# Kernel tuning notes

Hardware: AMD Instinct MI355X
Metric: run time of the kernel (lower is better)

Reference implementation:

```python
import jax, jax.numpy as jnp
import numpy as np

D_MODEL = 768
NUM_HEADS = 12
HEAD_DIM = D_MODEL // NUM_HEADS


def setup_inputs() -> dict:
    key = jax.random.key(0)
    ks = jax.random.split(key, 9)
    B, S = 2, 2048
    s = 1.0 / np.sqrt(D_MODEL)
    x = jax.random.normal(ks[0], (B, S, D_MODEL), dtype=jnp.float32)
    Wq = jax.random.normal(ks[1], (D_MODEL, D_MODEL), dtype=jnp.float32) * s
    Wk = jax.random.normal(ks[2], (D_MODEL, D_MODEL), dtype=jnp.float32) * s
    Wv = jax.random.normal(ks[3], (D_MODEL, D_MODEL), dtype=jnp.float32) * s
    Wo = jax.random.normal(ks[4], (D_MODEL, D_MODEL), dtype=jnp.float32) * s
    bq = jax.random.normal(ks[5], (D_MODEL,), dtype=jnp.float32) * 0.01
    bk = jax.random.normal(ks[6], (D_MODEL,), dtype=jnp.float32) * 0.01
    bv = jax.random.normal(ks[7], (D_MODEL,), dtype=jnp.float32) * 0.01
    bo = jax.random.normal(ks[8], (D_MODEL,), dtype=jnp.float32) * 0.01
    return {"x": x, "Wq": Wq, "bq": bq, "Wk": Wk, "bk": bk,
            "Wv": Wv, "bv": bv, "Wo": Wo, "bo": bo}


def reference(x, Wq, bq, Wk, bk, Wv, bv, Wo, bo):
    B, S, _ = x.shape
    # projections; reshape to [B, H, S, Dh]
    def split_heads(t):
        return t.reshape(B, S, NUM_HEADS, HEAD_DIM).transpose(0, 2, 1, 3)
    q = split_heads(x @ Wq + bq)
    k = split_heads(x @ Wk + bk)
    v = split_heads(x @ Wv + bv)
    scale = 1.0 / np.sqrt(HEAD_DIM)
    scores = jnp.einsum("bhqd,bhkd->bhqk", q, k) * scale  # [B,H,S,S]
    attn = jax.nn.softmax(scores, axis=-1)
    # dropout p=0.0 (eval) -> identity
    ctx = jnp.einsum("bhqk,bhkd->bhqd", attn, v)
    ctx = ctx.transpose(0, 2, 1, 3).reshape(B, S, D_MODEL)
    return ctx @ Wo + bo
```

## Files before the change

### kernel.cpp

```cpp
#include <hip/hip_runtime.h>
#include <hip/hip_bf16.h>
#include <hip/hip_fp16.h>

#define D_MODEL 768
#define NHEADS  12
#define HD      64
#define BATCH   2
#define SEQ     2048
#define NTOK    (BATCH*SEQ)
#define NX      ((size_t)NTOK * D_MODEL)
#define NW      ((size_t)D_MODEL * D_MODEL)
#define SC_LOG2 0.18033688f

typedef __attribute__((ext_vector_type(8))) short    short8;
typedef __attribute__((ext_vector_type(8))) _Float16 half8;
typedef __attribute__((ext_vector_type(2))) __fp16   fp16x2;
typedef __attribute__((ext_vector_type(4))) float    f32x4;

__device__ __forceinline__ float bf2f(short s) {
    union { unsigned u; float f; } c;
    c.u = ((unsigned)(unsigned short)s) << 16;
    return c.f;
}
__device__ __forceinline__ short f2bf(float f) {
    __hip_bfloat16 h = __float2bfloat16(f);
    return *(short*)&h;
}

#ifdef __has_builtin
#if __has_builtin(__builtin_amdgcn_global_load_lds)
#define HAS_GLD 1
#endif
#if __has_builtin(__builtin_amdgcn_exp2f)
#define EXP2(x) __builtin_amdgcn_exp2f(x)
#else
#define EXP2(x) exp2f(x)
#endif
#if __has_builtin(__builtin_amdgcn_cvt_pkrtz)
#define HAS_PKRTZ 1
#endif
#else
#define EXP2(x) exp2f(x)
#endif
#ifdef HAS_GLD
#define GLD16(gp, lp) __builtin_amdgcn_global_load_lds( \
    (const __attribute__((address_space(1))) void*)(gp), \
    (__attribute__((address_space(3))) void*)(lp), 16, 0, 0)
#endif

#ifdef HAS_PKRTZ
#define PKF16(a, b) __builtin_amdgcn_cvt_pkrtz((a), (b))
#else
#define PKF16(a, b) ((fp16x2){ (__fp16)(a), (__fp16)(b) })
#endif

__global__ __launch_bounds__(256) void fused_conv(
        const void* __restrict__ xin,
        const void* __restrict__ w0, const void* __restrict__ w1,
        const void* __restrict__ w2, const void* __restrict__ w3,
        const void* __restrict__ b0, const void* __restrict__ b1,
        const void* __restrict__ b2, const void* __restrict__ b3,
        short* __restrict__ xc, short* __restrict__ wt,
        short* __restrict__ bc, int* __restrict__ flag)
{
    __shared__ int red[256];
    __shared__ float T[64][65];
    const int tid = threadIdx.x;
    const int F = blockIdx.x;

    {
        const short* xs = (const short*)xin;
        int maxe = 0;
#pragma unroll
        for (int u = 0; u < 16; ++u) {
            int e = ((unsigned short)xs[tid * 16 + u] >> 7) & 0xFF;
            maxe = max(maxe, e);
        }
        red[tid] = maxe;
        __syncthreads();
        for (int s = 128; s > 0; s >>= 1) {
            if (tid < s) red[tid] = max(red[tid], red[tid + s]);
            __syncthreads();
        }
    }
    const bool isf = (red[0] > 140);

    if (F < 3072) {
        const int i = F * 256 + tid;
        if (isf) {
            float4 f = ((const float4*)xin)[i];
            short4 o = { f2bf(f.x), f2bf(f.y), f2bf(f.z), f2bf(f.w) };
            ((short4*)xc)[i] = o;
        } else {
            ((short4*)xc)[i] = ((const short4*)xin)[i];
        }
    } else if (F < 3648) {
        const int G = F - 3072;
        const int z = G / 144, rr = G % 144;
        const int k0 = (rr % 12) * 64, n0 = (rr / 12) * 64;
        const void* src = (z == 0) ? w0 : (z == 1) ? w1 : (z == 2) ? w2 : w3;
        const float sc = (z == 0) ? SC_LOG2 : 1.0f;
        const int la = tid & 15, lb = tid >> 4;
#pragma unroll
        for (int u = 0; u < 4; ++u) {
            const int kr = (lb & 3) + 4 * u + 16 * (lb >> 2);
            if (isf) {
                float4 f = *(const float4*)((const float*)src + (size_t)(k0 + kr) * D_MODEL + n0 + la * 4);
                T[kr][la*4+0] = f.x; T[kr][la*4+1] = f.y; T[kr][la*4+2] = f.z; T[kr][la*4+3] = f.w;
            } else {
                short4 s = *(const short4*)((const short*)src + (size_t)(k0 + kr) * D_MODEL + n0 + la * 4);
                T[kr][la*4+0] = bf2f(s.x); T[kr][la*4+1] = bf2f(s.y);
                T[kr][la*4+2] = bf2f(s.z); T[kr][la*4+3] = bf2f(s.w);
            }
        }
        __syncthreads();
#pragma unroll
        for (int u = 0; u < 4; ++u) {
            const int nr = (lb & 3) + 4 * u + 16 * (lb >> 2);
            short4 o = { f2bf(T[la*4+0][nr] * sc), f2bf(T[la*4+1][nr] * sc),
                         f2bf(T[la*4+2][nr] * sc), f2bf(T[la*4+3][nr] * sc) };
            *(short4*)(wt + (size_t)z * NW + (size_t)(n0 + nr) * D_MODEL + k0 + la * 4) = o;
        }
    } else {
        if (tid == 0) *flag = isf ? 1 : 0;
        const void* srcs[4] = { b0, b1, b2, b3 };
        for (int z = 0; z < 4; ++z) {
            const float sc = (z == 0) ? SC_LOG2 : 1.0f;
            for (int i = tid; i < D_MODEL; i += 256) {
                float v = isf ? ((const float*)srcs[z])[i] : bf2f(((const short*)srcs[z])[i]);
                bc[z * D_MODEL + i] = f2bf(v * sc);
            }
        }
    }
}

__global__ __launch_bounds__(256) void qkv_gemm(const short* __restrict__ X,
                                                const short* __restrict__ Wt,
                                                const short* __restrict__ bias,
                                                short* __restrict__ qb,
                                                short* __restrict__ kb,
                                                _Float16* __restrict__ Vt)
{
    __shared__ __align__(16) char shbuf[24576];
    short* Als = (short*)shbuf;
    short* Bls = (short*)(shbuf + 8192);
    _Float16* T = (_Float16*)shbuf;

    const int tid = threadIdx.x;
    const int wave = tid >> 6, lane = tid & 63;
    const int quad = lane >> 4, l16 = lane & 15;
    const int wm = wave & 1, wn = wave >> 1;
    const int m0 = blockIdx.x * 64;
    const int ng = blockIdx.y * 128;

    f32x4 acc[2][4];
#pragma unroll
    for (int nt = 0; nt < 4; ++nt) {
        const float bv = bf2f(bias[ng + wn*64 + nt*16 + l16]);
#pragma unroll
        for (int mt = 0; mt < 2; ++mt) acc[mt][nt] = (f32x4){bv, bv, bv, bv};
    }

    const int row = tid >> 2, ch = (tid & 3) * 8;
#ifdef HAS_GLD
#define QSTAGE(buf, k0) do { \
        GLD16(X  + (size_t)(m0 + row)      * D_MODEL + (k0) + ch, &Als[(buf)*2048 + tid*8]); \
        GLD16(Wt + (size_t)(ng + row)      * D_MODEL + (k0) + ch, &Bls[(buf)*4096 + tid*8]); \
        GLD16(Wt + (size_t)(ng + 64 + row) * D_MODEL + (k0) + ch, &Bls[(buf)*4096 + 2048 + tid*8]); \
    } while (0)
#else
#define QSTAGE(buf, k0) do { \
        short8 r0 = *(const short8*)(X  + (size_t)(m0 + row)      * D_MODEL + (k0) + ch); \
        short8 r2 = *(const short8*)(Wt + (size_t)(ng + row)      * D_MODEL + (k0) + ch); \
        short8 r3 = *(const short8*)(Wt + (size_t)(ng + 64 + row) * D_MODEL + (k0) + ch); \
        *(short8*)&Als[(buf)*2048 + tid*8] = r0; \
        *(short8*)&Bls[(buf)*4096 + tid*8] = r2; \
        *(short8*)&Bls[(buf)*4096 + 2048 + tid*8] = r3; \
    } while (0)
#endif

    QSTAGE(0, 0);
    __syncthreads();

    for (int ks = 0; ks < 24; ++ks) {
        const int cur = ks & 1;
        if (ks + 1 < 24) QSTAGE(cur ^ 1, (ks + 1) * 32);

        short8 a[2], b[4];
#pragma unroll
        for (int mt = 0; mt < 2; ++mt)
            a[mt] = *(const short8*)&Als[cur*2048 + (wm*32 + mt*16 + l16) * 32 + quad*8];
#pragma unroll
        for (int nt = 0; nt < 4; ++nt)
            b[nt] = *(const short8*)&Bls[cur*4096 + (wn*64 + nt*16 + l16) * 32 + quad*8];
#pragma unroll
        for (int mt = 0; mt < 2; ++mt)
#pragma unroll
        for (int nt = 0; nt < 4; ++nt)
            acc[mt][nt] = __builtin_amdgcn_mfma_f32_16x16x32_bf16(a[mt], b[nt], acc[mt][nt], 0, 0, 0);

        __syncthreads();
    }
#undef QSTAGE

    const int seg = blockIdx.y / 6;
    if (seg < 2) {
        short* out = seg ? kb : qb;
        const int nl = ng - seg * 768;
#pragma unroll
        for (int mt = 0; mt < 2; ++mt)
#pragma unroll
        for (int nt = 0; nt < 4; ++nt) {
            const int n = nl + wn*64 + nt*16 + l16;
#pragma unroll
            for (int r = 0; r < 4; ++r) {
                const int m = m0 + wm*32 + mt*16 + quad*4 + r;
                out[(size_t)m * D_MODEL + n] = f2bf(acc[mt][nt][r]);
            }
        }
    } else {
        const int batch = m0 >> 11, tokb = m0 & (SEQ - 1);
#pragma unroll
        for (int nt = 0; nt < 4; ++nt) {
            const int dim_l = wn*64 + nt*16 + l16;
#pragma unroll
            for (int mt = 0; mt < 2; ++mt) {
                const int tok_l = wm*32 + mt*16 + quad*4;
                union { _Float16 h4[4]; int2 v; } u;
#pragma unroll
                for (int r = 0; r < 4; ++r) u.h4[r] = (_Float16)acc[mt][nt][r];
                *(int2*)&T[dim_l * 72 + tok_l] = u.v;
            }
        }
        __syncthreads();
#pragma unroll
        for (int u = 0; u < 4; ++u) {
            const int slot = tid + u * 256;
            const int drow = slot >> 3, chk = slot & 7;
            int4 val = *(const int4*)&T[drow * 72 + chk * 8];
            const int dim_g = ng - 1536 + drow;
            const int h = dim_g >> 6, d = dim_g & 63;
            *(int4*)(Vt + ((size_t)(batch * NHEADS + h) * HD + d) * SEQ + tokb + chk*8) = val;
        }
    }
}

__global__ __launch_bounds__(256) void out_gemm(const short* __restrict__ X,
                                                const short* __restrict__ Wt,
                                                const short* __restrict__ bias,
                                                void* __restrict__ outv,
                                                const int* __restrict__ flag)
{
    __shared__ short Als[2][2048];
    __shared__ short Bls[2][2048];

    const int tid = threadIdx.x;
    const int wave = tid >> 6, lane = tid & 63;
    const int quad = lane >> 4, l16 = lane & 15;
    const int m0 = blockIdx.x * 64;
    const int n0 = blockIdx.y * 64;

    f32x4 acc[4];
#pragma unroll
    for (int nt = 0; nt < 4; ++nt) {
        const float bv = bf2f(bias[n0 + nt*16 + l16]);
        acc[nt] = (f32x4){bv, bv, bv, bv};
    }

    const int row = tid >> 2, ch = (tid & 3) * 8;
#ifdef HAS_GLD
#define OSTAGE(buf, k0) do { \
        GLD16(X  + (size_t)(m0 + row) * D_MODEL + (k0) + ch, &Als[buf][tid*8]); \
        GLD16(Wt + (size_t)(n0 + row) * D_MODEL + (k0) + ch, &Bls[buf][tid*8]); \
    } while (0)
#else
#define OSTAGE(buf, k0) do { \
        short8 r0 = *(const short8*)(X  + (size_t)(m0 + row) * D_MODEL + (k0) + ch); \
        short8 r1 = *(const short8*)(Wt + (size_t)(n0 + row) * D_MODEL + (k0) + ch); \
        *(short8*)&Als[buf][tid*8] = r0; \
        *(short8*)&Bls[buf][tid*8] = r1; \
    } while (0)
#endif

    OSTAGE(0, 0);
    __syncthreads();

    for (int ks = 0; ks < 24; ++ks) {
        const int cur = ks & 1;
        if (ks + 1 < 24) OSTAGE(cur ^ 1, (ks + 1) * 32);

        short8 a = *(const short8*)&Als[cur][(wave*16 + l16) * 32 + quad*8];
#pragma unroll
        for (int nt = 0; nt < 4; ++nt) {
            short8 b = *(const short8*)&Bls[cur][(nt*16 + l16) * 32 + quad*8];
            acc[nt] = __builtin_amdgcn_mfma_f32_16x16x32_bf16(a, b, acc[nt], 0, 0, 0);
        }
        __syncthreads();
    }
#undef OSTAGE

    const bool outf32 = (*flag != 0);
#pragma unroll
    for (int nt = 0; nt < 4; ++nt) {
        const int n = n0 + nt*16 + l16;
#pragma unroll
        for (int r = 0; r < 4; ++r) {
            const int m = m0 + wave*16 + quad*4 + r;
            const size_t idx = (size_t)m * D_MODEL + n;
            if (outf32) ((float*)outv)[idx] = acc[nt][r];
            else        ((short*)outv)[idx] = f2bf(acc[nt][r]);
        }
    }
}

__global__ __launch_bounds__(256, 3) void attn_mfma(const short* __restrict__ q,
                                                    const short* __restrict__ k,
                                                    const _Float16* __restrict__ Vt,
                                                    short* __restrict__ ctx)
{
    __shared__ short    Kls[2][64 * 64];
    __shared__ _Float16 Vls[3][64 * 64];
    __shared__ _Float16 Pls[4][16 * 64];

    const int tid  = threadIdx.x;
    const int wave = tid >> 6, lane = tid & 63;
    const int quad = lane >> 4, l16 = lane & 15;

    const int F = blockIdx.x;
    const int xcd = F & 7, slot = F >> 3;
    const int bh = xcd * 3 + (slot >> 5);
    const int q0 = (slot & 31) * 64;
    const int b = bh / NHEADS, h = bh % NHEADS;
    const size_t bS = (size_t)b * SEQ;
    const int myq = q0 + wave * 16 + l16;

    short8 qf[2];
#pragma unroll
    for (int k0h = 0; k0h < 2; ++k0h)
        qf[k0h] = *(const short8*)(q + (bS + myq) * D_MODEL + h*HD + k0h*32 + quad*8);

    half8 ones;
#pragma unroll
    for (int j = 0; j < 8; ++j) ones[j] = (_Float16)1.0f;

    const int s0 = tid, s1 = tid + 256;
    const int kr0 = s0 >> 3, kc0 = (s0 & 7) ^ (kr0 & 7);
    const int kr1 = s1 >> 3, kc1 = (s1 & 7) ^ (kr1 & 7);
    const short*    kg0 = k  + (bS + kr0) * D_MODEL + h*HD + kc0*8;
    const short*    kg1 = k  + (bS + kr1) * D_MODEL + h*HD + kc1*8;
    const _Float16* vg0 = Vt + ((size_t)bh * HD + kr0) * SEQ + kc0*8;
    const _Float16* vg1 = Vt + ((size_t)bh * HD + kr1) * SEQ + kc1*8;

#ifdef HAS_GLD
#define STAGE_K(buf, j0) do { \
        GLD16(kg0 + (size_t)(j0) * D_MODEL, &Kls[buf][s0 * 8]); \
        GLD16(kg1 + (size_t)(j0) * D_MODEL, &Kls[buf][s1 * 8]); \
    } while (0)
#define STAGE_V(buf, j0) do { \
        GLD16(vg0 + (j0), &Vls[buf][s0 * 8]); \
        GLD16(vg1 + (j0), &Vls[buf][s1 * 8]); \
    } while (0)
#else
#define STAGE_K(buf, j0) do { \
        short8 a_ = *(const short8*)(kg0 + (size_t)(j0) * D_MODEL); \
        short8 b_ = *(const short8*)(kg1 + (size_t)(j0) * D_MODEL); \
        *(short8*)&Kls[buf][s0 * 8] = a_;  *(short8*)&Kls[buf][s1 * 8] = b_; \
    } while (0)
#define STAGE_V(buf, j0) do { \
        half8  c_ = *(const half8*)(vg0 + (j0)); \
        half8  d_ = *(const half8*)(vg1 + (j0)); \
        *(half8*)&Vls[buf][s0 * 8] = c_;   *(half8*)&Vls[buf][s1 * 8] = d_; \
    } while (0)
#endif

    float m_ = -1e30f;
    f32x4 lacc = (f32x4){0.f, 0.f, 0.f, 0.f};
    f32x4 o[4];
#pragma unroll
    for (int t = 0; t < 4; ++t) o[t] = (f32x4){0.f, 0.f, 0.f, 0.f};

    f32x4 sA[4], sB[4];

#define QK(S, KB) do { \
    _Pragma("unroll") \
    for (int t = 0; t < 4; ++t) S[t] = (f32x4){0.f, 0.f, 0.f, 0.f}; \
    _Pragma("unroll") \
    for (int k0h = 0; k0h < 2; ++k0h) \
    _Pragma("unroll") \
    for (int t = 0; t < 4; ++t) { \
        const int krow = t*16 + l16; \
        short8 kf = *(const short8*)&Kls[KB][krow*64 + (((k0h*4 + quad) ^ (krow & 7)) * 8)]; \
        S[t] = __builtin_amdgcn_mfma_f32_16x16x32_bf16(kf, qf[k0h], S[t], 0, 0, 0); \
    } \
} while (0)

#define BODY(JT, SCUR, SNXT) do { \
    if ((JT) + 2 < SEQ/64) { \
        STAGE_K(((JT) + 2) & 1, ((JT) + 2) * 64); \
        STAGE_V(((JT) + 2) % 3, ((JT) + 2) * 64); \
    } \
    if ((JT) + 1 < SEQ/64) QK(SNXT, ((JT) + 1) & 1); \
    { \
         \
        float mx = SCUR[0][0]; \
        _Pragma("unroll") \
        for (int t = 0; t < 4; ++t) \
        _Pragma("unroll") \
        for (int r = 0; r < 4; ++r) mx = fmaxf(mx, SCUR[t][r]); \
        if (__any(mx > m_ + 8.f)) { \
            _Pragma("unroll") \
            for (int d = 1; d < 64; d <<= 1) mx = fmaxf(mx, __shfl_xor(mx, d)); \
            const float mn = fmaxf(m_, mx); \
            const float al = EXP2(m_ - mn); \
            _Pragma("unroll") \
            for (int t = 0; t < 4; ++t) { \
                o[t][0] *= al; o[t][1] *= al; o[t][2] *= al; o[t][3] *= al; \
            } \
            lacc[0] *= al; lacc[1] *= al; lacc[2] *= al; lacc[3] *= al; \
            m_ = mn; \
        } \
         \
        _Pragma("unroll") \
        for (int t = 0; t < 4; ++t) { \
            union { fp16x2 h2[2]; int2 v; } u4; \
            u4.h2[0] = PKF16(EXP2(SCUR[t][0] - m_), EXP2(SCUR[t][1] - m_)); \
            u4.h2[1] = PKF16(EXP2(SCUR[t][2] - m_), EXP2(SCUR[t][3] - m_)); \
            const int c = (t*2 + (quad >> 1)) ^ (l16 & 7); \
            *(int2*)&Pls[wave][l16*64 + c*8 + (quad & 1)*4] = u4.v; \
        } \
         \
        const int vb = (JT) % 3; \
        _Pragma("unroll") \
        for (int k0h = 0; k0h < 2; ++k0h) { \
            const int pc = (k0h*4 + quad) ^ (l16 & 7); \
            half8 pf = *(half8*)&Pls[wave][l16*64 + pc*8]; \
            lacc = __builtin_amdgcn_mfma_f32_16x16x32_f16(ones, pf, lacc, 0, 0, 0); \
            _Pragma("unroll") \
            for (int t = 0; t < 4; ++t) { \
                const int vrow = t*16 + l16; \
                half8 vf = *(const half8*)&Vls[vb][vrow*64 + (((k0h*4 + quad) ^ (vrow & 7)) * 8)]; \
                o[t] = __builtin_amdgcn_mfma_f32_16x16x32_f16(vf, pf, o[t], 0, 0, 0); \
            } \
        } \
    } \
    __syncthreads(); \
} while (0)

    STAGE_K(0, 0); STAGE_V(0, 0);
    __syncthreads();
    STAGE_K(1, 64); STAGE_V(1, 64);
    QK(sA, 0);
    __syncthreads();

    for (int jt = 0; jt < SEQ / 64; jt += 2) {
        BODY(jt,     sA, sB);
        BODY(jt + 1, sB, sA);
    }

    const float inv = 1.0f / lacc[0];
    const size_t rowp = (bS + myq) * D_MODEL + h*HD;
#pragma unroll
    for (int t = 0; t < 4; ++t) {
        union { short s4v[4]; int2 v; } u4;
#pragma unroll
        for (int r = 0; r < 4; ++r) u4.s4v[r] = f2bf(o[t][r] * inv);
        *(int2*)(ctx + rowp + t*16 + quad*4) = u4.v;
    }
#undef BODY
#undef QK
#undef STAGE_K
#undef STAGE_V
}

extern "C" void kernel_launch(void* const* d_in, const int* in_sizes, int n_in,
                              void* d_out, int out_size, void* d_ws, size_t ws_size,
                              hipStream_t stream)
{
    int* flag = (int*)d_ws;
    short* xc = (short*)((char*)d_ws + 64);
    short* Wt = xc + NX;
    short* bc = Wt + 4 * NW;
    short* qb = bc + 4 * D_MODEL;
    short* kb = qb + NX;
    _Float16* Vt = (_Float16*)(kb + NX);
    short* cb = (short*)(Vt + NX);

    fused_conv<<<3649, 256, 0, stream>>>(d_in[0],
                                         d_in[1], d_in[3], d_in[5], d_in[7],
                                         d_in[2], d_in[4], d_in[6], d_in[8],
                                         xc, Wt, bc, flag);

    qkv_gemm<<<dim3(NTOK/64, 2304/128), 256, 0, stream>>>(xc, Wt, bc, qb, kb, Vt);

    attn_mfma<<<768, 256, 0, stream>>>(qb, kb, Vt, cb);

    out_gemm<<<dim3(NTOK/64, D_MODEL/64), 256, 0, stream>>>(cb, Wt + 3*NW, bc + 3*D_MODEL, d_out, flag);
}
```

Baseline: 174.1 us.

## Split attention over key halves with 32-key tiles and add combine kernel

The attention kernel now splits each query block's key range into two halves (flash-decoding style), doubling the grid to 1536 blocks. It uses 32-key tiles with a new non-swizzled LDS layout, raises launch bounds occupancy to 6, and adds s_setprio around the MFMA sections. Each half writes partial fp16 outputs plus running max and sum, and a new combine kernel merges them into the bf16 context. This adds extra global traffic and a kernel launch in exchange for more parallelism and occupancy. The new LDS layout may also bring bank conflicts.

Result: slower. 189.8 us (+9.0%).

```diff
diff --git a/kernel.cpp b/kernel.cpp
--- a/kernel.cpp
+++ b/kernel.cpp
@@ -10,6 +10,7 @@
 #define NTOK    (BATCH*SEQ)
 #define NX      ((size_t)NTOK * D_MODEL)
 #define NW      ((size_t)D_MODEL * D_MODEL)
+#define NBH     (BATCH*NHEADS)
 #define SC_LOG2 0.18033688f
 
 typedef __attribute__((ext_vector_type(8))) short    short8;
@@ -313,14 +314,15 @@
     }
 }
 
-__global__ __launch_bounds__(256, 3) void attn_mfma(const short* __restrict__ q,
+__global__ __launch_bounds__(256, 6) void attn_mfma(const short* __restrict__ q,
                                                     const short* __restrict__ k,
                                                     const _Float16* __restrict__ Vt,
-                                                    short* __restrict__ ctx)
+                                                    _Float16* __restrict__ Op,
+                                                    float* __restrict__ mlp)
 {
-    __shared__ short    Kls[2][64 * 64];
-    __shared__ _Float16 Vls[3][64 * 64];
-    __shared__ _Float16 Pls[4][16 * 64];
+    __shared__ short    Kls[2][2048];
+    __shared__ _Float16 Vls[3][2048];
+    __shared__ _Float16 Pls[4][512];
 
     const int tid  = threadIdx.x;
     const int wave = tid >> 6, lane = tid & 63;
@@ -328,8 +330,11 @@
 
     const int F = blockIdx.x;
     const int xcd = F & 7, slot = F >> 3;
-    const int bh = xcd * 3 + (slot >> 5);
-    const int q0 = (slot & 31) * 64;
+    const int bh = xcd * 3 + (slot >> 6);
+    const int rem = slot & 63;
+    const int q0 = (rem >> 1) * 64;
+    const int sp = rem & 1;
+    const int kb0 = sp * (SEQ / 2);
     const int b = bh / NHEADS, h = bh % NHEADS;
     const size_t bS = (size_t)b * SEQ;
     const int myq = q0 + wave * 16 + l16;
@@ -343,34 +348,21 @@
 #pragma unroll
     for (int j = 0; j < 8; ++j) ones[j] = (_Float16)1.0f;
 
-    const int s0 = tid, s1 = tid + 256;
-    const int kr0 = s0 >> 3, kc0 = (s0 & 7) ^ (kr0 & 7);
-    const int kr1 = s1 >> 3, kc1 = (s1 & 7) ^ (kr1 & 7);
-    const short*    kg0 = k  + (bS + kr0) * D_MODEL + h*HD + kc0*8;
-    const short*    kg1 = k  + (bS + kr1) * D_MODEL + h*HD + kc1*8;
-    const _Float16* vg0 = Vt + ((size_t)bh * HD + kr0) * SEQ + kc0*8;
-    const _Float16* vg1 = Vt + ((size_t)bh * HD + kr1) * SEQ + kc1*8;
+    const int cK = tid >> 5, keyK = tid & 31;
+    const int cV = tid >> 6, dimV = tid & 63;
+    const short*    kgp = k  + (bS + kb0 + keyK) * D_MODEL + h*HD + cK*8;
+    const _Float16* vgp = Vt + ((size_t)bh * HD + dimV) * SEQ + kb0 + cV*8;
 
 #ifdef HAS_GLD
-#define STAGE_K(buf, j0) do { \
-        GLD16(kg0 + (size_t)(j0) * D_MODEL, &Kls[buf][s0 * 8]); \
-        GLD16(kg1 + (size_t)(j0) * D_MODEL, &Kls[buf][s1 * 8]); \
-    } while (0)
-#define STAGE_V(buf, j0) do { \
-        GLD16(vg0 + (j0), &Vls[buf][s0 * 8]); \
-        GLD16(vg1 + (j0), &Vls[buf][s1 * 8]); \
-    } while (0)
+#define STAGE_K(buf, j0) GLD16(kgp + (size_t)(j0) * D_MODEL, &Kls[buf][tid*8])
+#define STAGE_V(buf, j0) GLD16(vgp + (j0),                   &Vls[buf][tid*8])
 #else
 #define STAGE_K(buf, j0) do { \
-        short8 a_ = *(const short8*)(kg0 + (size_t)(j0) * D_MODEL); \
-        short8 b_ = *(const short8*)(kg1 + (size_t)(j0) * D_MODEL); \
-        *(short8*)&Kls[buf][s0 * 8] = a_;  *(short8*)&Kls[buf][s1 * 8] = b_; \
-    } while (0)
+        short8 a_ = *(const short8*)(kgp + (size_t)(j0) * D_MODEL); \
+        *(short8*)&Kls[buf][tid*8] = a_; } while (0)
 #define STAGE_V(buf, j0) do { \
-        half8  c_ = *(const half8*)(vg0 + (j0)); \
-        half8  d_ = *(const half8*)(vg1 + (j0)); \
-        *(half8*)&Vls[buf][s0 * 8] = c_;   *(half8*)&Vls[buf][s1 * 8] = d_; \
-    } while (0)
+        half8 c_ = *(const half8*)(vgp + (j0)); \
+        *(half8*)&Vls[buf][tid*8] = c_; } while (0)
 #endif
 
     float m_ = -1e30f;
@@ -379,32 +371,34 @@
 #pragma unroll
     for (int t = 0; t < 4; ++t) o[t] = (f32x4){0.f, 0.f, 0.f, 0.f};
 
-    f32x4 sA[4], sB[4];
+    f32x4 sA[2], sB[2];
+
+#define NT (SEQ / 2 / 32)
 
 #define QK(S, KB) do { \
-    _Pragma("unroll") \
-    for (int t = 0; t < 4; ++t) S[t] = (f32x4){0.f, 0.f, 0.f, 0.f}; \
+    S[0] = (f32x4){0.f,0.f,0.f,0.f}; S[1] = (f32x4){0.f,0.f,0.f,0.f}; \
+    __builtin_amdgcn_s_setprio(1); \
     _Pragma("unroll") \
     for (int k0h = 0; k0h < 2; ++k0h) \
     _Pragma("unroll") \
-    for (int t = 0; t < 4; ++t) { \
-        const int krow = t*16 + l16; \
-        short8 kf = *(const short8*)&Kls[KB][krow*64 + (((k0h*4 + quad) ^ (krow & 7)) * 8)]; \
+    for (int t = 0; t < 2; ++t) { \
+        short8 kf = *(const short8*)&Kls[KB][(k0h*4 + quad)*256 + (t*16 + l16)*8]; \
         S[t] = __builtin_amdgcn_mfma_f32_16x16x32_bf16(kf, qf[k0h], S[t], 0, 0, 0); \
     } \
+    __builtin_amdgcn_s_setprio(0); \
 } while (0)
 
 #define BODY(JT, SCUR, SNXT) do { \
-    if ((JT) + 2 < SEQ/64) { \
-        STAGE_K(((JT) + 2) & 1, ((JT) + 2) * 64); \
-        STAGE_V(((JT) + 2) % 3, ((JT) + 2) * 64); \
+    if ((JT) + 2 < NT) { \
+        STAGE_K(((JT) + 2) & 1, ((JT) + 2) * 32); \
+        STAGE_V(((JT) + 2) % 3, ((JT) + 2) * 32); \
     } \
-    if ((JT) + 1 < SEQ/64) QK(SNXT, ((JT) + 1) & 1); \
+    if ((JT) + 1 < NT) QK(SNXT, ((JT) + 1) & 1); \
     { \
          \
         float mx = SCUR[0][0]; \
         _Pragma("unroll") \
-        for (int t = 0; t < 4; ++t) \
+        for (int t = 0; t < 2; ++t) \
         _Pragma("unroll") \
         for (int r = 0; r < 4; ++r) mx = fmaxf(mx, SCUR[t][r]); \
         if (__any(mx > m_ + 8.f)) { \
@@ -416,60 +410,86 @@
             for (int t = 0; t < 4; ++t) { \
                 o[t][0] *= al; o[t][1] *= al; o[t][2] *= al; o[t][3] *= al; \
             } \
-            lacc[0] *= al; lacc[1] *= al; lacc[2] *= al; lacc[3] *= al; \
+            lacc[0] *= al; \
             m_ = mn; \
         } \
          \
         _Pragma("unroll") \
-        for (int t = 0; t < 4; ++t) { \
+        for (int t = 0; t < 2; ++t) { \
             union { fp16x2 h2[2]; int2 v; } u4; \
             u4.h2[0] = PKF16(EXP2(SCUR[t][0] - m_), EXP2(SCUR[t][1] - m_)); \
             u4.h2[1] = PKF16(EXP2(SCUR[t][2] - m_), EXP2(SCUR[t][3] - m_)); \
-            const int c = (t*2 + (quad >> 1)) ^ (l16 & 7); \
-            *(int2*)&Pls[wave][l16*64 + c*8 + (quad & 1)*4] = u4.v; \
+            const int c = 2*t + (quad >> 1); \
+            *(int2*)&Pls[wave][c*128 + l16*8 + (quad & 1)*4] = u4.v; \
         } \
          \
         const int vb = (JT) % 3; \
+        half8 pf = *(half8*)&Pls[wave][quad*128 + l16*8]; \
+        __builtin_amdgcn_s_setprio(1); \
+        lacc = __builtin_amdgcn_mfma_f32_16x16x32_f16(ones, pf, lacc, 0, 0, 0); \
         _Pragma("unroll") \
-        for (int k0h = 0; k0h < 2; ++k0h) { \
-            const int pc = (k0h*4 + quad) ^ (l16 & 7); \
-            half8 pf = *(half8*)&Pls[wave][l16*64 + pc*8]; \
-            lacc = __builtin_amdgcn_mfma_f32_16x16x32_f16(ones, pf, lacc, 0, 0, 0); \
-            _Pragma("unroll") \
-            for (int t = 0; t < 4; ++t) { \
-                const int vrow = t*16 + l16; \
-                half8 vf = *(const half8*)&Vls[vb][vrow*64 + (((k0h*4 + quad) ^ (vrow & 7)) * 8)]; \
-                o[t] = __builtin_amdgcn_mfma_f32_16x16x32_f16(vf, pf, o[t], 0, 0, 0); \
-            } \
+        for (int t = 0; t < 4; ++t) { \
+            half8 vf = *(const half8*)&Vls[vb][quad*512 + (t*16 + l16)*8]; \
+            o[t] = __builtin_amdgcn_mfma_f32_16x16x32_f16(vf, pf, o[t], 0, 0, 0); \
         } \
+        __builtin_amdgcn_s_setprio(0); \
     } \
     __syncthreads(); \
 } while (0)
 
     STAGE_K(0, 0); STAGE_V(0, 0);
     __syncthreads();
-    STAGE_K(1, 64); STAGE_V(1, 64);
+    STAGE_K(1, 32); STAGE_V(1, 32);
     QK(sA, 0);
     __syncthreads();
 
-    for (int jt = 0; jt < SEQ / 64; jt += 2) {
+    for (int jt = 0; jt < NT; jt += 2) {
         BODY(jt,     sA, sB);
         BODY(jt + 1, sB, sA);
     }
 
     const float inv = 1.0f / lacc[0];
-    const size_t rowp = (bS + myq) * D_MODEL + h*HD;
+    const size_t prow = ((size_t)sp * (NBH * SEQ) + (size_t)bh * SEQ + myq);
+    _Float16* orow = Op + prow * HD;
 #pragma unroll
     for (int t = 0; t < 4; ++t) {
-        union { short s4v[4]; int2 v; } u4;
-#pragma unroll
-        for (int r = 0; r < 4; ++r) u4.s4v[r] = f2bf(o[t][r] * inv);
-        *(int2*)(ctx + rowp + t*16 + quad*4) = u4.v;
+        union { _Float16 h4[4]; int2 v; } u4;
+#pragma unroll
+        for (int r = 0; r < 4; ++r) u4.h4[r] = (_Float16)(o[t][r] * inv);
+        *(int2*)(orow + t*16 + quad*4) = u4.v;
+    }
+    if (quad == 0) {
+        float2 mlv; mlv.x = m_; mlv.y = lacc[0];
+        *(float2*)&mlp[prow * 2] = mlv;
     }
 #undef BODY
 #undef QK
+#undef NT
 #undef STAGE_K
 #undef STAGE_V
+}
+
+__global__ __launch_bounds__(256) void attn_combine(const _Float16* __restrict__ Op,
+                                                    const float* __restrict__ mlp,
+                                                    short* __restrict__ ctx)
+{
+    const int gid = blockIdx.x * 256 + threadIdx.x;
+    const int r = gid >> 3, seg = gid & 7;
+    const float2 a  = *(const float2*)&mlp[(size_t)r * 2];
+    const float2 c2 = *(const float2*)&mlp[((size_t)(NBH * SEQ) + r) * 2];
+    const float M  = fmaxf(a.x, c2.x);
+    const float w1 = EXP2(a.x - M) * a.y;
+    const float w2 = EXP2(c2.x - M) * c2.y;
+    const float inv = 1.0f / (w1 + w2);
+    const half8 o1 = *(const half8*)&Op[(size_t)r * HD + seg * 8];
+    const half8 o2 = *(const half8*)&Op[(size_t)(NBH * SEQ) * HD + (size_t)r * HD + seg * 8];
+    union { short s[8]; int4 v; } u;
+#pragma unroll
+    for (int j = 0; j < 8; ++j)
+        u.s[j] = f2bf((w1 * (float)o1[j] + w2 * (float)o2[j]) * inv);
+    const int bh = r >> 11, qq = r & (SEQ - 1);
+    const int bb = bh / NHEADS, hh = bh % NHEADS;
+    *(int4*)&ctx[((size_t)(bb * SEQ + qq)) * D_MODEL + hh * HD + seg * 8] = u.v;
 }
 
 extern "C" void kernel_launch(void* const* d_in, const int* in_sizes, int n_in,
@@ -484,6 +504,8 @@
     short* kb = qb + NX;
     _Float16* Vt = (_Float16*)(kb + NX);
     short* cb = (short*)(Vt + NX);
+    _Float16* Op = (_Float16*)(cb + NX);
+    float* mlp = (float*)(Op + (size_t)2 * NBH * SEQ * HD);
 
     fused_conv<<<3649, 256, 0, stream>>>(d_in[0],
                                          d_in[1], d_in[3], d_in[5], d_in[7],
@@ -492,7 +514,9 @@
 
     qkv_gemm<<<dim3(NTOK/64, 2304/128), 256, 0, stream>>>(xc, Wt, bc, qb, kb, Vt);
 
-    attn_mfma<<<768, 256, 0, stream>>>(qb, kb, Vt, cb);
+    attn_mfma<<<1536, 256, 0, stream>>>(qb, kb, Vt, Op, mlp);
+
+    attn_combine<<<1536, 256, 0, stream>>>(Op, mlp, cb);
 
     out_gemm<<<dim3(NTOK/64, D_MODEL/64), 256, 0, stream>>>(cb, Wt + 3*NW, bc + 3*D_MODEL, d_out, flag);
 }
```
